# Optimization experiments

Measured on AMD Instinct MI355X. Metric: run time of the kernel, lower is better.

Reference implementation:

```python
import jax, jax.numpy as jnp
import numpy as np

SEQ_LEN = 2048
EMBED_DIM = 1024
NUM_HEADS = 16
DIM_HEAD = EMBED_DIM // NUM_HEADS
BATCH = 4


def setup_inputs() -> dict:
    key = jax.random.key(0)
    k1, k2, k3 = jax.random.split(key, 3)
    x = jax.random.normal(k1, (SEQ_LEN, BATCH, EMBED_DIM), dtype=jnp.float32)
    weight_qkv = jax.random.normal(k2, (3 * EMBED_DIM, EMBED_DIM), dtype=jnp.float32) * (EMBED_DIM ** -0.5)
    weight_out = jax.random.normal(k3, (EMBED_DIM, EMBED_DIM), dtype=jnp.float32) * (EMBED_DIM ** -0.5)
    # causal mask: True where attention is DISALLOWED (strict upper triangle)
    mask = ~jnp.tril(jnp.ones((SEQ_LEN, SEQ_LEN), dtype=bool))[None, None]  # [1,1,L,L]
    return {"x": x, "weight_qkv": weight_qkv, "weight_out": weight_out, "mask": mask}


def reference(x, weight_qkv, weight_out, mask):
    L, N, E = x.shape
    H, Dh = NUM_HEADS, DIM_HEAD
    scale = Dh ** -0.5
    qkv = x @ weight_qkv.T                       # [L, N, 3E]
    q, k, v = jnp.split(qkv, 3, axis=-1)         # each [L, N, E]
    # [L, N, E] -> [N*H, L, Dh]
    def to_heads(t):
        return t.reshape(L, N * H, Dh).transpose(1, 0, 2)
    q, k, v = to_heads(q) * scale, to_heads(k), to_heads(v)
    attn = jnp.einsum('bld,bmd->blm', q, k)      # [N*H, L, L]
    attn = attn.reshape(N, H, L, L)
    attn = jnp.where(mask, jnp.float32(-100000.0), attn)
    attn = jax.nn.softmax(attn.reshape(N * H, L, L), axis=-1)
    out = jnp.einsum('blm,bmd->bld', attn, v)    # [N*H, L, Dh]
    out = out.transpose(1, 0, 2).reshape(L, N, E)
    return out @ weight_out.T
```

## Files before the change

kernel.cpp:

```cpp
#include <hip/hip_runtime.h>
#include <hip/hip_bf16.h>
#include <stdint.h>

constexpr int L  = 2048;
constexpr int NB = 4;
constexpr int E  = 1024;
constexpr int H  = 16;
constexpr int M  = L * NB;
constexpr int K  = E;
constexpr int QKV_LD = 3 * E;

typedef float  f32x4  __attribute__((ext_vector_type(4)));
typedef float  f32x16 __attribute__((ext_vector_type(16)));
typedef __bf16 bf16x4 __attribute__((ext_vector_type(4)));
typedef __bf16 bf16x8 __attribute__((ext_vector_type(8)));
typedef unsigned int uint2v __attribute__((ext_vector_type(2)));
typedef unsigned int uint4v __attribute__((ext_vector_type(4)));

#define AS1 __attribute__((address_space(1)))
#define AS3 __attribute__((address_space(3)))

static __device__ __forceinline__ void gl_lds16(const void* g, void* l) {
  __builtin_amdgcn_global_load_lds((const AS1 uint32_t*)g, (AS3 uint32_t*)l, 16, 0, 0);
}

__global__ __launch_bounds__(256)
void cvt_all(const float* __restrict__ x, const float* __restrict__ wq,
             const float* __restrict__ wo, __bf16* __restrict__ xb,
             __bf16* __restrict__ wqb, __bf16* __restrict__ wob) {
  const int bid = blockIdx.x;
  const float* src;
  __bf16* dst;
  int i;
  if (bid < 8192)        { src = x;  dst = xb;  i = bid * 256 + threadIdx.x; }
  else if (bid < 11264)  { src = wq; dst = wqb; i = (bid - 8192) * 256 + threadIdx.x; }
  else                   { src = wo; dst = wob; i = (bid - 11264) * 256 + threadIdx.x; }
  const f32x4 v = ((const f32x4*)src)[i];
  bf16x4 o;
#pragma unroll
  for (int j = 0; j < 4; j++) o[j] = (__bf16)v[j];
  ((bf16x4*)dst)[i] = o;
}

template<int NC, typename OutT>
__global__ __launch_bounds__(256)
void gemm_bt(const __bf16* __restrict__ A, const __bf16* __restrict__ B,
             OutT* __restrict__ C) {
  constexpr int BK = 64;
  __shared__ char lds[2 * 128 * BK * 2];
  char* aL = lds;
  char* bL = lds + 128 * BK * 2;

  const int t    = threadIdx.x;
  const int lane = t & 63;
  const int w    = t >> 6;
  const int g    = lane >> 4;
  const int c    = lane & 15;

  const int nwg = gridDim.x * gridDim.y;
  const int lin = blockIdx.x + gridDim.x * blockIdx.y;
  const int q8  = nwg >> 3;
  const int swz = (lin & 7) * q8 + (lin >> 3);
  const int bx  = swz % gridDim.x;
  const int by  = swz / gridDim.x;

  const int rowBase = by * 128;
  const int colBase = bx * 128;

  const int srow = t >> 3;
  const int scb  = (t & 7) * 16;
  const int ssw  = scb ^ ((srow & 7) << 4);

  const char* aSrcBase = (const char*)(A + (size_t)(rowBase + srow) * K) + ssw;
  const char* bSrcBase = (const char*)(B + (size_t)(colBase + srow) * K) + ssw;

  f32x4 acc[4][4];
#pragma unroll
  for (int i = 0; i < 4; i++)
#pragma unroll
    for (int j = 0; j < 4; j++) acc[i][j] = f32x4{0.f, 0.f, 0.f, 0.f};

  const int wr = (w >> 1) * 64;
  const int wc = (w & 1) * 64;

  for (int k0 = 0; k0 < K; k0 += BK) {
    __syncthreads();
#pragma unroll
    for (int q = 0; q < 4; q++) {
      gl_lds16(aSrcBase + (size_t)2 * k0 + (size_t)q * 32 * K * 2, aL + q * 4096 + t * 16);
      gl_lds16(bSrcBase + (size_t)2 * k0 + (size_t)q * 32 * K * 2, bL + q * 4096 + t * 16);
    }
    __syncthreads();

    bf16x8 af[4][2], bfR[4][2];
#pragma unroll
    for (int mi = 0; mi < 4; mi++) {
      const int row = wr + mi * 16 + c;
      const int sw  = (row & 7) << 4;
#pragma unroll
      for (int ks = 0; ks < 2; ks++)
        af[mi][ks] = *(const bf16x8*)(aL + row * 128 + ((ks * 64 + g * 16) ^ sw));
    }
#pragma unroll
    for (int ni = 0; ni < 4; ni++) {
      const int row = wc + ni * 16 + c;
      const int sw  = (row & 7) << 4;
#pragma unroll
      for (int ks = 0; ks < 2; ks++)
        bfR[ni][ks] = *(const bf16x8*)(bL + row * 128 + ((ks * 64 + g * 16) ^ sw));
    }
#pragma unroll
    for (int mi = 0; mi < 4; mi++)
#pragma unroll
      for (int ni = 0; ni < 4; ni++)
#pragma unroll
        for (int ks = 0; ks < 2; ks++)
          acc[mi][ni] = __builtin_amdgcn_mfma_f32_16x16x32_bf16(
              af[mi][ks], bfR[ni][ks], acc[mi][ni], 0, 0, 0);
  }

#pragma unroll
  for (int mi = 0; mi < 4; mi++)
#pragma unroll
    for (int ni = 0; ni < 4; ni++)
#pragma unroll
      for (int r = 0; r < 4; r++) {
        const int row = rowBase + wr + mi * 16 + g * 4 + r;
        const int col = colBase + wc + ni * 16 + c;
        C[(size_t)row * NC + col] = (OutT)acc[mi][ni][r];
      }
}

__global__ __launch_bounds__(256)
void transpose_v(const __bf16* __restrict__ qkv, __bf16* __restrict__ vT) {
  __shared__ char tile[64 * 160];
  const int lt = blockIdx.x;
  const int bh = blockIdx.y;
  const int n  = bh >> 4, h = bh & 15;
  const int t  = threadIdx.x;
  const int r8 = t >> 3;
  const int c8 = (t & 7) * 8;

#pragma unroll
  for (int q2 = 0; q2 < 2; q2++) {
    const int l = q2 * 32 + r8;
    const bf16x8 v = *(const bf16x8*)(qkv + (size_t)((lt * 64 + l) * 4 + n) * QKV_LD +
                                      2 * E + h * 64 + c8);
    *(bf16x8*)(tile + l * 160 + ((c8 * 2) ^ (((l >> 3) & 7) << 4))) = v;
  }
  __syncthreads();
#pragma unroll
  for (int q2 = 0; q2 < 2; q2++) {
    const int d = q2 * 32 + r8;
    bf16x8 o;
#pragma unroll
    for (int i = 0; i < 8; i++) {
      const int l = c8 + i;
      o[i] = *(const __bf16*)(tile + l * 160 + ((d * 2) ^ (((l >> 3) & 7) << 4)));
    }
    *(bf16x8*)(vT + ((size_t)bh * 64 + d) * 2048 + lt * 64 + c8) = o;
  }
}

__global__ __launch_bounds__(128)
void attn_kernel(const __bf16* __restrict__ qkv, const __bf16* __restrict__ vT,
                 __bf16* __restrict__ out) {
  const int b   = blockIdx.x;
  const int sup = 31 - (int)blockIdx.y;
  const int n   = b >> 4;
  const int h   = b & 15;

  __shared__ char kl[64 * 128];
  __shared__ char vl[64 * 128];

  const int t    = threadIdx.x;
  const int lane = t & 63;
  const int w    = t >> 6;
  const int l31  = lane & 31;
  const int hi   = lane >> 5;

  const int srow = t >> 3;
  const int scb  = (t & 7) * 16;
  int kssw[4];
#pragma unroll
  for (int q2 = 0; q2 < 4; q2++) {
    const int row = q2 * 16 + srow;
    kssw[q2] = scb ^ (((row ^ (row >> 3)) & 7) << 4);
  }

  const int krow0 = l31,      sw0 = ((krow0 ^ (krow0 >> 3)) & 7) << 4;
  const int krow1 = 32 + l31, sw1 = ((krow1 ^ (krow1 >> 3)) & 7) << 4;

  constexpr float QSCALE = 0.125f * 1.4426950408889634f;

  const int qb_ = sup * 64 + w * 32;
  const int qg  = qb_ + l31;

  bf16x8 qb[4];
  {
    const __bf16* qp = qkv + (size_t)(qg * 4 + n) * QKV_LD + h * 64;
#pragma unroll
    for (int ds = 0; ds < 4; ds++) {
      qb[ds] = *(const bf16x8*)(qp + ds * 16 + hi * 8);
#pragma unroll
      for (int i = 0; i < 8; i++) qb[ds][i] = (__bf16)((float)qb[ds][i] * QSCALE);
    }
  }

  float m_c = -3e38f, l_c = 0.f;
  f32x16 o0, o1;
#pragma unroll
  for (int j = 0; j < 16; j++) { o0[j] = 0.f; o1[j] = 0.f; }

  for (int kt = 0; kt <= sup; ++kt) {
    __syncthreads();
#pragma unroll
    for (int q2 = 0; q2 < 4; q2++) {
      const int kvrow = kt * 64 + q2 * 16 + srow;
      gl_lds16((const char*)(qkv + (size_t)(kvrow * 4 + n) * QKV_LD + E + h * 64) + kssw[q2],
               kl + q2 * 2048 + t * 16);
      const int vd = q2 * 16 + srow;
      gl_lds16((const char*)(vT + ((size_t)b * 64 + vd) * 2048 + kt * 64) + kssw[q2],
               vl + q2 * 2048 + t * 16);
    }
    __syncthreads();

    f32x16 s0, s1;
#pragma unroll
    for (int j = 0; j < 16; j++) { s0[j] = 0.f; s1[j] = 0.f; }
    __builtin_amdgcn_s_setprio(1);
#pragma unroll
    for (int ds = 0; ds < 4; ds++) {
      const int col = ds * 32 + hi * 16;
      const bf16x8 ka0 = *(const bf16x8*)(kl + krow0 * 128 + (col ^ sw0));
      const bf16x8 ka1 = *(const bf16x8*)(kl + krow1 * 128 + (col ^ sw1));
      s0 = __builtin_amdgcn_mfma_f32_32x32x16_bf16(ka0, qb[ds], s0, 0, 0, 0);
      s1 = __builtin_amdgcn_mfma_f32_32x32x16_bf16(ka1, qb[ds], s1, 0, 0, 0);
    }
    __builtin_amdgcn_s_setprio(0);

    if (kt == sup) {
#pragma unroll
      for (int reg = 0; reg < 16; reg++) {
        const int kvp = (reg & 3) + 8 * (reg >> 2) + 4 * hi;
        if (kt * 64 + kvp      > qg) s0[reg] = -1e30f;
        if (kt * 64 + 32 + kvp > qg) s1[reg] = -1e30f;
      }
    }

    float rmax = s0[0];
#pragma unroll
    for (int reg = 1; reg < 16; reg++) rmax = fmaxf(rmax, s0[reg]);
#pragma unroll
    for (int reg = 0; reg < 16; reg++) rmax = fmaxf(rmax, s1[reg]);
    rmax = fmaxf(rmax, __shfl_xor(rmax, 32));

    if (__any(rmax > m_c + 8.f)) {
      const float mnew  = fmaxf(m_c, rmax);
      const float alpha = exp2f(m_c - mnew);
      l_c *= alpha;
#pragma unroll
      for (int reg = 0; reg < 16; reg++) {
        const int   qp = (reg & 3) + 8 * (reg >> 2) + 4 * hi;
        const float ar = __shfl(alpha, qp);
        o0[reg] *= ar;
        o1[reg] *= ar;
      }
      m_c = mnew;
    }

    float rsum = 0.f;
#pragma unroll
    for (int reg = 0; reg < 16; reg++) {
      const float e0 = exp2f(s0[reg] - m_c);
      const float e1 = exp2f(s1[reg] - m_c);
      s0[reg] = e0; s1[reg] = e1;
      rsum += e0 + e1;
    }
    rsum += __shfl_xor(rsum, 32);
    l_c += rsum;

    unsigned int runA[8], runB[8];
#pragma unroll
    for (int rg = 0; rg < 8; rg++) {
      bf16x4 pk;
#pragma unroll
      for (int j = 0; j < 4; j++)
        pk[j] = (__bf16)((rg < 4) ? s0[(rg & 3) * 4 + j] : s1[(rg & 3) * 4 + j]);
      const uint2v u = *(const uint2v*)&pk;
      runA[rg] = u[0]; runB[rg] = u[1];
    }

#pragma unroll
    for (int s_ = 0; s_ < 4; s_++) {
      const unsigned int ownA = hi ? runA[2 * s_ + 1] : runA[2 * s_];
      const unsigned int ownB = hi ? runB[2 * s_ + 1] : runB[2 * s_];
      const unsigned int sndA = hi ? runA[2 * s_]     : runA[2 * s_ + 1];
      const unsigned int sndB = hi ? runB[2 * s_]     : runB[2 * s_ + 1];
      const unsigned int rxA  = (unsigned int)__shfl_xor((int)sndA, 32);
      const unsigned int rxB  = (unsigned int)__shfl_xor((int)sndB, 32);
      uint4v pu;
      pu[0] = hi ? rxA : ownA;  pu[1] = hi ? rxB : ownB;
      pu[2] = hi ? ownA : rxA;  pu[3] = hi ? ownB : rxB;
      const bf16x8 pa = *(const bf16x8*)&pu;

      const int colp = s_ * 32 + hi * 16;
      const bf16x8 vb0 = *(const bf16x8*)(vl + krow0 * 128 + (colp ^ sw0));
      const bf16x8 vb1 = *(const bf16x8*)(vl + krow1 * 128 + (colp ^ sw1));
      __builtin_amdgcn_s_setprio(1);
      o0 = __builtin_amdgcn_mfma_f32_32x32x16_bf16(pa, vb0, o0, 0, 0, 0);
      o1 = __builtin_amdgcn_mfma_f32_32x32x16_bf16(pa, vb1, o1, 0, 0, 0);
      __builtin_amdgcn_s_setprio(0);
    }
  }

  const float inv = 1.f / l_c;
#pragma unroll
  for (int reg = 0; reg < 16; reg++) {
    const int   qp  = (reg & 3) + 8 * (reg >> 2) + 4 * hi;
    const float li  = __shfl(inv, qp);
    const int   qrw = qb_ + qp;
    const size_t base = (size_t)(qrw * 4 + n) * E + h * 64;
    out[base + l31]      = (__bf16)(o0[reg] * li);
    out[base + 32 + l31] = (__bf16)(o1[reg] * li);
  }
}

extern "C" void kernel_launch(void* const* d_in, const int* in_sizes, int n_in,
                              void* d_out, int out_size, void* d_ws, size_t ws_size,
                              hipStream_t stream) {
  const float* x    = (const float*)d_in[0];
  const float* wqkv = (const float*)d_in[1];
  const float* wout = (const float*)d_in[2];

  char* ws = (char*)d_ws;
  __bf16* x_bf    = (__bf16*)ws;                         ws += (size_t)M * E * 2;
  __bf16* wqkv_bf = (__bf16*)ws;                         ws += (size_t)QKV_LD * E * 2;
  __bf16* wout_bf = (__bf16*)ws;                         ws += (size_t)E * E * 2;
  __bf16* qkv     = (__bf16*)ws;                         ws += (size_t)M * QKV_LD * 2;
  __bf16* attno   = (__bf16*)ws;
  __bf16* vT      = x_bf;
  float*  outp    = (float*)d_out;

  cvt_all<<<12288, 256, 0, stream>>>(x, wqkv, wout, x_bf, wqkv_bf, wout_bf);

  gemm_bt<QKV_LD, __bf16><<<dim3(QKV_LD / 128, M / 128), 256, 0, stream>>>(x_bf, wqkv_bf, qkv);
  transpose_v<<<dim3(L / 64, NB * H), 256, 0, stream>>>(qkv, vT);
  attn_kernel<<<dim3(NB * H, 32), 128, 0, stream>>>(qkv, vT, attno);
  gemm_bt<E, float><<<dim3(E / 128, M / 128), 256, 0, stream>>>(attno, wout_bf, outp);
}
```

Measured before the change: 192.8 us.

## Double-buffer K/V tiles in LDS to prefetch the next tile during compute

The attention kernel's K and V shared-memory tiles become double buffers. The first tile is loaded before the loop, and each iteration issues async global-to-LDS loads for the next tile before computing on the current one. This drops one of the two barriers per iteration and aims to hide global load latency behind the MFMA and softmax work. LDS use per block doubles, which may lower occupancy. The compiler may also insert conservative vmcnt waits before the LDS reads, which would limit the overlap.

```diff
diff --git a/kernel.cpp b/kernel.cpp
--- a/kernel.cpp
+++ b/kernel.cpp
@@ -170,8 +170,8 @@
   const int n   = b >> 4;
   const int h   = b & 15;
 
-  __shared__ char kl[64 * 128];
-  __shared__ char vl[64 * 128];
+  __shared__ char kl[2][64 * 128];
+  __shared__ char vl[2][64 * 128];
 
   const int t    = threadIdx.x;
   const int lane = t & 63;
@@ -212,18 +212,36 @@
 #pragma unroll
   for (int j = 0; j < 16; j++) { o0[j] = 0.f; o1[j] = 0.f; }
 
+  int cur = 0;
+
+#pragma unroll
+  for (int q2 = 0; q2 < 4; q2++) {
+    const int kvrow = q2 * 16 + srow;
+    gl_lds16((const char*)(qkv + (size_t)(kvrow * 4 + n) * QKV_LD + E + h * 64) + kssw[q2],
+             kl[0] + q2 * 2048 + t * 16);
+    gl_lds16((const char*)(vT + ((size_t)b * 64 + q2 * 16 + srow) * 2048) + kssw[q2],
+             vl[0] + q2 * 2048 + t * 16);
+  }
+
   for (int kt = 0; kt <= sup; ++kt) {
     __syncthreads();
-#pragma unroll
-    for (int q2 = 0; q2 < 4; q2++) {
-      const int kvrow = kt * 64 + q2 * 16 + srow;
-      gl_lds16((const char*)(qkv + (size_t)(kvrow * 4 + n) * QKV_LD + E + h * 64) + kssw[q2],
-               kl + q2 * 2048 + t * 16);
-      const int vd = q2 * 16 + srow;
-      gl_lds16((const char*)(vT + ((size_t)b * 64 + vd) * 2048 + kt * 64) + kssw[q2],
-               vl + q2 * 2048 + t * 16);
-    }
-    __syncthreads();
+
+    if (kt < sup) {
+      const int nx = kt + 1;
+#pragma unroll
+      for (int q2 = 0; q2 < 4; q2++) {
+        const int kvrow = nx * 64 + q2 * 16 + srow;
+        gl_lds16((const char*)(qkv + (size_t)(kvrow * 4 + n) * QKV_LD + E + h * 64) + kssw[q2],
+                 kl[cur ^ 1] + q2 * 2048 + t * 16);
+        const int vd = q2 * 16 + srow;
+        gl_lds16((const char*)(vT + ((size_t)b * 64 + vd) * 2048 + nx * 64) + kssw[q2],
+                 vl[cur ^ 1] + q2 * 2048 + t * 16);
+      }
+    }
+    __builtin_amdgcn_sched_barrier(0);
+
+    const char* klc = kl[cur];
+    const char* vlc = vl[cur];
 
     f32x16 s0, s1;
 #pragma unroll
@@ -232,8 +250,8 @@
 #pragma unroll
     for (int ds = 0; ds < 4; ds++) {
       const int col = ds * 32 + hi * 16;
-      const bf16x8 ka0 = *(const bf16x8*)(kl + krow0 * 128 + (col ^ sw0));
-      const bf16x8 ka1 = *(const bf16x8*)(kl + krow1 * 128 + (col ^ sw1));
+      const bf16x8 ka0 = *(const bf16x8*)(klc + krow0 * 128 + (col ^ sw0));
+      const bf16x8 ka1 = *(const bf16x8*)(klc + krow1 * 128 + (col ^ sw1));
       s0 = __builtin_amdgcn_mfma_f32_32x32x16_bf16(ka0, qb[ds], s0, 0, 0, 0);
       s1 = __builtin_amdgcn_mfma_f32_32x32x16_bf16(ka1, qb[ds], s1, 0, 0, 0);
     }
@@ -305,13 +323,15 @@
       const bf16x8 pa = *(const bf16x8*)&pu;
 
       const int colp = s_ * 32 + hi * 16;
-      const bf16x8 vb0 = *(const bf16x8*)(vl + krow0 * 128 + (colp ^ sw0));
-      const bf16x8 vb1 = *(const bf16x8*)(vl + krow1 * 128 + (colp ^ sw1));
+      const bf16x8 vb0 = *(const bf16x8*)(vlc + krow0 * 128 + (colp ^ sw0));
+      const bf16x8 vb1 = *(const bf16x8*)(vlc + krow1 * 128 + (colp ^ sw1));
       __builtin_amdgcn_s_setprio(1);
       o0 = __builtin_amdgcn_mfma_f32_32x32x16_bf16(pa, vb0, o0, 0, 0, 0);
       o1 = __builtin_amdgcn_mfma_f32_32x32x16_bf16(pa, vb1, o1, 0, 0, 0);
       __builtin_amdgcn_s_setprio(0);
     }
+
+    cur ^= 1;
   }
 
   const float inv = 1.f / l_c;
```

New measurement: 193.6 us. Within noise of the previous version (+0.4%).
